# Performance work log

Hardware: AMD Instinct MI355X
Metric: run time of the kernel (lower is better)

## Reference

```python
import jax, jax.numpy as jnp
import numpy as np

B = 4096
IN_FEATS = 1024
OUT_FEATS = 1024
NUM_HEADS = 16
NUM_MEMS = 4096
HEAD_DIM = OUT_FEATS // NUM_HEADS
TEMPERATURE = 1.0
EPS = 0.0  # original code uses plain jnp.linalg.norm (no eps)


def setup_inputs() -> dict:
    key = jax.random.key(0)
    k1, k2, k3 = jax.random.split(key, 3)
    x = jax.random.normal(k1, (B, IN_FEATS), dtype=jnp.float32)
    # eqx.nn.Linear stores weight as [out, in]; uniform-like init replaced with normal scaled
    W_q = jax.random.normal(k2, (OUT_FEATS, IN_FEATS), dtype=jnp.float32) * (1.0 / np.sqrt(IN_FEATS))
    memories = jax.random.normal(k3, (NUM_HEADS, NUM_MEMS, HEAD_DIM), dtype=jnp.float32) * 0.02
    return {"x": x, "W_q": W_q, "memories": memories}


def reference(x, W_q, memories):
    # q = query_proj(x): [B, out_feats] -> [B, H, d]
    q = (x @ W_q.T).reshape(B, NUM_HEADS, HEAD_DIM)
    # L2-normalize queries and memories along feature dim
    q_norm = q / jnp.linalg.norm(q, axis=-1, keepdims=True)
    mem_norm = memories / jnp.linalg.norm(memories, axis=-1, keepdims=True)
    # cosine-similarity scores: [B, H, M]
    attn_scores = jnp.einsum('bhd,hmd->bhm', q_norm, mem_norm)
    # soft readout (hard=False branch)
    mem_probs = jax.nn.softmax(attn_scores / TEMPERATURE, axis=-1)
    # weighted combine of normalized memories, scaled by sqrt(head_dim)
    out = jnp.einsum('bhm,hmd->bhd', mem_probs, mem_norm) * jnp.sqrt(HEAD_DIM).astype(x.dtype)
    return out.reshape(B, OUT_FEATS)
```

## Files before the change

### kernel.cpp

```cpp
#include <hip/hip_runtime.h>
#include <stdint.h>

#define B_SZ  4096
#define HEADS 16
#define HD    64
#define M_SZ  4096
#define K_IN  1024
#define SW    72
#define LOG2E 1.44269504088896f

typedef _Float16 f16;
typedef f16  f16x4 __attribute__((ext_vector_type(4)));
typedef f16  f16x8 __attribute__((ext_vector_type(8)));
typedef float f32x4 __attribute__((ext_vector_type(4)));

union U8 { uint4 u4; f16x8 h8; unsigned int ui[4]; unsigned short us[8]; };

__device__ __forceinline__ unsigned short f2h(float f) {
    _Float16 h = (_Float16)f;
    return __builtin_bit_cast(unsigned short, h);
}
__device__ __forceinline__ f16x8 ldsv8(const unsigned short* p) {
    U8 u; u.u4 = *reinterpret_cast<const uint4*>(p); return u.h8;
}

#if __has_builtin(__builtin_amdgcn_exp2f)
#define EXP2F(x) __builtin_amdgcn_exp2f(x)
#else
#define EXP2F(x) __expf((x) * 0.6931471805599453f)
#endif

__device__ __forceinline__ void gload_lds16(const void* g, void* l) {
    __builtin_amdgcn_global_load_lds(
        (const __attribute__((address_space(1))) void*)g,
        (__attribute__((address_space(3))) void*)l, 16, 0, 0);
}

__global__ __launch_bounds__(256) void k_conv(const float* __restrict__ x,
                                              const float* __restrict__ Wq,
                                              unsigned short* __restrict__ xh,
                                              unsigned short* __restrict__ Wh) {
    const int b = blockIdx.x;
    const float* src;
    unsigned short* dst;
    size_t base;
    if (b < 2048) { src = x;  dst = xh; base = (size_t)b * 2048; }
    else          { src = Wq; dst = Wh; base = (size_t)(b - 2048) * 2048; }
    const size_t i = base + (size_t)threadIdx.x * 8;
    float4 f0 = reinterpret_cast<const float4*>(src + i)[0];
    float4 f1 = reinterpret_cast<const float4*>(src + i)[1];
    U8 u;
    u.us[0] = f2h(f0.x); u.us[1] = f2h(f0.y); u.us[2] = f2h(f0.z); u.us[3] = f2h(f0.w);
    u.us[4] = f2h(f1.x); u.us[5] = f2h(f1.y); u.us[6] = f2h(f1.z); u.us[7] = f2h(f1.w);
    *reinterpret_cast<uint4*>(dst + i) = u.u4;
}

__global__ __launch_bounds__(256) void k_prep_mem(const float* __restrict__ mem,
                                                  unsigned short* __restrict__ F) {
    __shared__ float part[64][4];
    __shared__ float scale[64];
    __shared__ unsigned short Tn[64 * SW];

    const int h  = blockIdx.y;
    const int tl = blockIdx.x;
    const int m0 = tl * 64;
    const int tid = threadIdx.x;
    const int r = tid >> 2;
    const int c = tid & 3;

    const float* src = mem + ((size_t)(h * M_SZ + m0 + r)) * HD + c * 16;
    float v[16];
    float ss = 0.f;
#pragma unroll
    for (int i = 0; i < 4; i++) {
        float4 f = reinterpret_cast<const float4*>(src)[i];
        v[4*i+0] = f.x; v[4*i+1] = f.y; v[4*i+2] = f.z; v[4*i+3] = f.w;
        ss += f.x*f.x + f.y*f.y + f.z*f.z + f.w*f.w;
    }
    part[r][c] = ss;
    __syncthreads();
    if (tid < 64) {
        float s = part[tid][0] + part[tid][1] + part[tid][2] + part[tid][3];
        scale[tid] = rsqrtf(s);
    }
    __syncthreads();
    const float sc = scale[r];

    U8 a, b;
#pragma unroll
    for (int i = 0; i < 8; i++) { a.us[i] = f2h(v[i] * sc); b.us[i] = f2h(v[8 + i] * sc); }
    *reinterpret_cast<uint4*>(&Tn[r * SW + c * 16])     = a.u4;
    *reinterpret_cast<uint4*>(&Tn[r * SW + c * 16 + 8]) = b.u4;
    __syncthreads();

    const int w = tid >> 6, lane = tid & 63;
    const int l15 = lane & 15, quad = lane >> 4;
    unsigned short* Fd = F + ((size_t)(h * 64 + tl) * 16) * 512;

#pragma unroll
    for (int i = 0; i < 2; i++) {
        const int ch = w * 2 + i, g = ch >> 1, s = ch & 1;
        const int mp = 32 * (g >> 1) + ((l15 >> 2) * 8) + 4 * (g & 1) + (l15 & 3);
        uint4 vv = *reinterpret_cast<const uint4*>(&Tn[mp * SW + s * 32 + quad * 8]);
        *reinterpret_cast<uint4*>(Fd + ch * 512 + lane * 8) = vv;
    }
#pragma unroll
    for (int i = 0; i < 2; i++) {
        const int c2 = w * 2 + i, p = c2 >> 2, n = c2 & 3;
        U8 u;
#pragma unroll
        for (int j = 0; j < 8; j++)
            u.us[j] = Tn[(32 * p + quad * 8 + j) * SW + n * 16 + l15];
        *reinterpret_cast<uint4*>(Fd + (8 + c2) * 512 + lane * 8) = u.u4;
    }
}

__global__ __launch_bounds__(256, 2) void k_qproj(const unsigned short* __restrict__ xh,
                                                  const unsigned short* __restrict__ Wh,
                                                  unsigned short* __restrict__ qn) {
    __shared__ unsigned short As[128 * SW];
    __shared__ unsigned short Bs[64 * SW];

    const int b0 = blockIdx.x * 128;
    const int n0 = blockIdx.y * 64;
    const int t = threadIdx.x;
    const int w = t >> 6, lane = t & 63;
    const int l15 = lane & 15, quad = lane >> 4;

    f32x4 acc[2][4] = {};

    for (int kb = 0; kb < K_IN; kb += 64) {
        __syncthreads();
        {
            const unsigned short* px = xh + (size_t)(b0 + (t >> 1)) * K_IN + kb + (t & 1) * 32;
            const unsigned short* pw = Wh + (size_t)(n0 + (t >> 2)) * K_IN + kb + (t & 3) * 16;
            uint4 av[4];
#pragma unroll
            for (int i = 0; i < 4; i++) av[i] = reinterpret_cast<const uint4*>(px)[i];
            uint4 bv[2];
#pragma unroll
            for (int i = 0; i < 2; i++) bv[i] = reinterpret_cast<const uint4*>(pw)[i];
#pragma unroll
            for (int i = 0; i < 4; i++)
                *reinterpret_cast<uint4*>(&As[(t >> 1) * SW + (t & 1) * 32 + i * 8]) = av[i];
#pragma unroll
            for (int i = 0; i < 2; i++)
                *reinterpret_cast<uint4*>(&Bs[(t >> 2) * SW + (t & 3) * 16 + i * 8]) = bv[i];
        }
        __syncthreads();

#pragma unroll
        for (int s = 0; s < 2; s++) {
            f16x8 af[2];
#pragma unroll
            for (int qg = 0; qg < 2; qg++)
                af[qg] = ldsv8(&As[(w * 32 + qg * 16 + l15) * SW + s * 32 + quad * 8]);
#pragma unroll
            for (int g = 0; g < 4; g++) {
                f16x8 bf_ = ldsv8(&Bs[(g * 16 + l15) * SW + s * 32 + quad * 8]);
#pragma unroll
                for (int qg = 0; qg < 2; qg++)
                    acc[qg][g] = __builtin_amdgcn_mfma_f32_16x16x32_f16(af[qg], bf_, acc[qg][g], 0, 0, 0);
            }
        }
    }

    __syncthreads();
    unsigned short* Ct = As;
#pragma unroll
    for (int qg = 0; qg < 2; qg++) {
        float ssq[4];
#pragma unroll
        for (int r = 0; r < 4; r++) {
            float s = 0.f;
#pragma unroll
            for (int g = 0; g < 4; g++) s += acc[qg][g][r] * acc[qg][g][r];
            ssq[r] = s;
        }
#pragma unroll
        for (int mask = 1; mask <= 8; mask <<= 1)
#pragma unroll
            for (int r = 0; r < 4; r++) ssq[r] += __shfl_xor(ssq[r], mask, 64);
#pragma unroll
        for (int r = 0; r < 4; r++) {
            float inv = rsqrtf(ssq[r]) * LOG2E;
#pragma unroll
            for (int g = 0; g < 4; g++)
                Ct[(w * 32 + qg * 16 + quad * 4 + r) * SW + g * 16 + l15] = f2h(acc[qg][g][r] * inv);
        }
    }
    __syncthreads();

    const int row = t >> 1, half = (t & 1) * 32;
    unsigned short* dq = qn + (size_t)(b0 + row) * 1024 + n0 + half;
#pragma unroll
    for (int i = 0; i < 4; i++)
        reinterpret_cast<uint4*>(dq)[i] = *reinterpret_cast<const uint4*>(&Ct[row * SW + half + i * 8]);
}

__global__ __launch_bounds__(256, 2) void k_attn(const unsigned short* __restrict__ qn,
                                                 const unsigned short* __restrict__ F,
                                                 float* __restrict__ out) {
    __shared__ unsigned short buf[2][8192];

    const int b = blockIdx.x;
    const int h  = 2 * (b & 7) + (b >> 8);
    const int b0 = ((b >> 3) & 31) * 128;
    const int t = threadIdx.x;
    const int w = t >> 6, lane = t & 63;
    const int l15 = lane & 15, quad = lane >> 4;

    f16x8 qf[2][2];
#pragma unroll
    for (int qg = 0; qg < 2; qg++)
#pragma unroll
        for (int s = 0; s < 2; s++) {
            U8 u;
            u.u4 = *reinterpret_cast<const uint4*>(
                qn + (size_t)(b0 + w * 32 + qg * 16 + l15) * 1024 + h * 64 + s * 32 + quad * 8);
            qf[qg][s] = u.h8;
        }

    const unsigned short* Fh = F + (size_t)h * 64 * 8192;

    f32x4 accO[2][4] = {};
    float lsum[2] = {0.f, 0.f};

    f16x8 puA[2][2], puB[2][2];
    f16x8 bwA[8],   bwB[8];

#pragma unroll
    for (int i = 0; i < 4; i++) {
        const int ch = w * 4 + i;
        gload_lds16(Fh + ch * 512 + lane * 8, &buf[0][ch * 512]);
    }
    __syncthreads();
    {
        f16x8 am[8];
#pragma unroll
        for (int ch = 0; ch < 8; ch++) am[ch] = ldsv8(&buf[0][ch * 512 + lane * 8]);
#pragma unroll
        for (int ch = 0; ch < 8; ch++) bwA[ch] = ldsv8(&buf[0][(8 + ch) * 512 + lane * 8]);
#pragma unroll
        for (int i = 0; i < 4; i++) {
            const int ch = w * 4 + i;
            gload_lds16(Fh + 8192 + ch * 512 + lane * 8, &buf[1][ch * 512]);
        }
#pragma unroll
        for (int g = 0; g < 4; g++) {
            const int qg = g >> 1, p = g & 1;
            f32x4 t0 = {0.f,0.f,0.f,0.f}, t1 = {0.f,0.f,0.f,0.f};
            t0 = __builtin_amdgcn_mfma_f32_16x16x32_f16(am[4*p+0], qf[qg][0], t0, 0, 0, 0);
            t0 = __builtin_amdgcn_mfma_f32_16x16x32_f16(am[4*p+1], qf[qg][1], t0, 0, 0, 0);
            t1 = __builtin_amdgcn_mfma_f32_16x16x32_f16(am[4*p+2], qf[qg][0], t1, 0, 0, 0);
            t1 = __builtin_amdgcn_mfma_f32_16x16x32_f16(am[4*p+3], qf[qg][1], t1, 0, 0, 0);
            float p0 = EXP2F(t0[0]), p1 = EXP2F(t0[1]), p2 = EXP2F(t0[2]), p3 = EXP2F(t0[3]);
            float p4 = EXP2F(t1[0]), p5 = EXP2F(t1[1]), p6 = EXP2F(t1[2]), p7 = EXP2F(t1[3]);
            lsum[qg] += ((p0 + p1) + (p2 + p3)) + ((p4 + p5) + (p6 + p7));
            U8 pu;
#if __has_builtin(__builtin_amdgcn_cvt_pkrtz)
            pu.ui[0] = __builtin_bit_cast(unsigned int, __builtin_amdgcn_cvt_pkrtz(p0, p1));
            pu.ui[1] = __builtin_bit_cast(unsigned int, __builtin_amdgcn_cvt_pkrtz(p2, p3));
            pu.ui[2] = __builtin_bit_cast(unsigned int, __builtin_amdgcn_cvt_pkrtz(p4, p5));
            pu.ui[3] = __builtin_bit_cast(unsigned int, __builtin_amdgcn_cvt_pkrtz(p6, p7));
#else
            pu.us[0]=f2h(p0); pu.us[1]=f2h(p1); pu.us[2]=f2h(p2); pu.us[3]=f2h(p3);
            pu.us[4]=f2h(p4); pu.us[5]=f2h(p5); pu.us[6]=f2h(p6); pu.us[7]=f2h(p7);
#endif
            puA[qg][p] = pu.h8;
        }
    }

    auto body = [&](int tl, f16x8 (&puC)[2][2], f16x8 (&bwC)[8],
                            f16x8 (&puN)[2][2], f16x8 (&bwN)[8]) {
        __syncthreads();
        const unsigned short* lb = buf[(tl + 1) & 1];
        f16x8 amn[8];
#pragma unroll
        for (int ch = 0; ch < 8; ch++) amn[ch] = ldsv8(&lb[ch * 512 + lane * 8]);
#pragma unroll
        for (int ch = 0; ch < 8; ch++) bwN[ch] = ldsv8(&lb[(8 + ch) * 512 + lane * 8]);
        if (tl + 2 < 64) {
            const unsigned short* gsrc = Fh + (size_t)(tl + 2) * 8192;
#pragma unroll
            for (int i = 0; i < 4; i++) {
                const int ch = w * 4 + i;
                gload_lds16(gsrc + ch * 512 + lane * 8, &buf[tl & 1][ch * 512]);
            }
        }

        f32x4 sa[4], sb[4];
        auto expPack = [&](int g) {
            const int qg = g >> 1, p = g & 1;
            float p0 = EXP2F(sa[g][0]), p1 = EXP2F(sa[g][1]), p2 = EXP2F(sa[g][2]), p3 = EXP2F(sa[g][3]);
            float p4 = EXP2F(sb[g][0]), p5 = EXP2F(sb[g][1]), p6 = EXP2F(sb[g][2]), p7 = EXP2F(sb[g][3]);
            lsum[qg] += ((p0 + p1) + (p2 + p3)) + ((p4 + p5) + (p6 + p7));
            U8 pu;
#if __has_builtin(__builtin_amdgcn_cvt_pkrtz)
            pu.ui[0] = __builtin_bit_cast(unsigned int, __builtin_amdgcn_cvt_pkrtz(p0, p1));
            pu.ui[1] = __builtin_bit_cast(unsigned int, __builtin_amdgcn_cvt_pkrtz(p2, p3));
            pu.ui[2] = __builtin_bit_cast(unsigned int, __builtin_amdgcn_cvt_pkrtz(p4, p5));
            pu.ui[3] = __builtin_bit_cast(unsigned int, __builtin_amdgcn_cvt_pkrtz(p6, p7));
#else
            pu.us[0]=f2h(p0); pu.us[1]=f2h(p1); pu.us[2]=f2h(p2); pu.us[3]=f2h(p3);
            pu.us[4]=f2h(p4); pu.us[5]=f2h(p5); pu.us[6]=f2h(p6); pu.us[7]=f2h(p7);
#endif
            puN[qg][p] = pu.h8;
        };

#pragma unroll
        for (int g = 0; g < 4; g++) {
            const int qg = g >> 1, p = g & 1;
            f32x4 t0 = {0.f,0.f,0.f,0.f}, t1 = {0.f,0.f,0.f,0.f};
            t0 = __builtin_amdgcn_mfma_f32_16x16x32_f16(amn[4*p+0], qf[qg][0], t0, 0, 0, 0);
            t0 = __builtin_amdgcn_mfma_f32_16x16x32_f16(amn[4*p+1], qf[qg][1], t0, 0, 0, 0);
            t1 = __builtin_amdgcn_mfma_f32_16x16x32_f16(amn[4*p+2], qf[qg][0], t1, 0, 0, 0);
            t1 = __builtin_amdgcn_mfma_f32_16x16x32_f16(amn[4*p+3], qf[qg][1], t1, 0, 0, 0);
            sa[g] = t0; sb[g] = t1;
#pragma unroll
            for (int n = 0; n < 4; n++)
                accO[qg][n] = __builtin_amdgcn_mfma_f32_16x16x32_f16(puC[qg][p], bwC[p * 4 + n], accO[qg][n], 0, 0, 0);
            if (g >= 1) expPack(g - 1);
        }
        expPack(3);
    };

    for (int tt = 0; tt < 31; ++tt) {
        body(2 * tt,     puA, bwA, puB, bwB);
        body(2 * tt + 1, puB, bwB, puA, bwA);
    }
    body(62, puA, bwA, puB, bwB);

#pragma unroll
    for (int g = 0; g < 4; g++) {
        const int qg = g >> 1, p = g & 1;
#pragma unroll
        for (int n = 0; n < 4; n++)
            accO[qg][n] = __builtin_amdgcn_mfma_f32_16x16x32_f16(puB[qg][p], bwB[p * 4 + n], accO[qg][n], 0, 0, 0);
    }

#pragma unroll
    for (int qg = 0; qg < 2; qg++) {
        float s = lsum[qg];
        s += __shfl_xor(s, 16, 64);
        s += __shfl_xor(s, 32, 64);
        float inv = 8.0f / s;
#pragma unroll
        for (int r = 0; r < 4; r++) {
            float iv = __shfl(inv, quad * 4 + r, 64);
            float* po = out + (size_t)(b0 + w * 32 + qg * 16 + quad * 4 + r) * 1024 + h * 64;
#pragma unroll
            for (int n = 0; n < 4; n++)
                po[n * 16 + l15] = accO[qg][n][r] * iv;
        }
    }
}

extern "C" void kernel_launch(void* const* d_in, const int* in_sizes, int n_in,
                              void* d_out, int out_size, void* d_ws, size_t ws_size,
                              hipStream_t stream) {
    (void)in_sizes; (void)n_in; (void)out_size; (void)ws_size;
    const float* x   = (const float*)d_in[0];
    const float* Wq  = (const float*)d_in[1];
    const float* mem = (const float*)d_in[2];
    float* out = (float*)d_out;

    unsigned short* qn = (unsigned short*)d_ws;
    unsigned short* F  = qn + (size_t)B_SZ * 1024;
    unsigned short* xh = F  + (size_t)HEADS * 64 * 16 * 512;
    unsigned short* Wh = xh + (size_t)B_SZ * K_IN;

    k_conv    <<<2560, 256, 0, stream>>>(x, Wq, xh, Wh);
    k_prep_mem<<<dim3(64, 16), 256, 0, stream>>>(mem, F);
    k_qproj   <<<dim3(32, 16), 256, 0, stream>>>(xh, Wh, qn);
    k_attn    <<<512, 256, 0, stream>>>(qn, F, out);
}
```

Measured before the change: 174.5 us.

## Use 8 waves per attention block with one 16-row query group each

The attention kernel now launches 512 threads per block instead of 256, and each wave handles 16 query rows instead of 32. Per-wave register state (accumulators, probabilities, query fragments) is halved. The F tile loads are spread over twice as many waves, and occupancy is raised via launch bounds (512, 4). The aim is more latency hiding through more concurrent waves. In exchange, every wave reloads the full F tile from LDS, so LDS read traffic per useful MFMA doubles, and the larger block synchronises more waves at each barrier.

After: 186.3 us. +6.8%, slower.

```diff
diff --git a/kernel.cpp b/kernel.cpp
--- a/kernel.cpp
+++ b/kernel.cpp
@@ -198,7 +198,7 @@
         reinterpret_cast<uint4*>(dq)[i] = *reinterpret_cast<const uint4*>(&Ct[row * SW + half + i * 8]);
 }
 
-__global__ __launch_bounds__(256, 2) void k_attn(const unsigned short* __restrict__ qn,
+__global__ __launch_bounds__(512, 4) void k_attn(const unsigned short* __restrict__ qn,
                                                  const unsigned short* __restrict__ F,
                                                  float* __restrict__ out) {
     __shared__ unsigned short buf[2][8192];
@@ -210,28 +210,26 @@
     const int w = t >> 6, lane = t & 63;
     const int l15 = lane & 15, quad = lane >> 4;
 
-    f16x8 qf[2][2];
-#pragma unroll
-    for (int qg = 0; qg < 2; qg++)
-#pragma unroll
-        for (int s = 0; s < 2; s++) {
-            U8 u;
-            u.u4 = *reinterpret_cast<const uint4*>(
-                qn + (size_t)(b0 + w * 32 + qg * 16 + l15) * 1024 + h * 64 + s * 32 + quad * 8);
-            qf[qg][s] = u.h8;
-        }
+    f16x8 qf[2];
+#pragma unroll
+    for (int s = 0; s < 2; s++) {
+        U8 u;
+        u.u4 = *reinterpret_cast<const uint4*>(
+            qn + (size_t)(b0 + w * 16 + l15) * 1024 + h * 64 + s * 32 + quad * 8);
+        qf[s] = u.h8;
+    }
 
     const unsigned short* Fh = F + (size_t)h * 64 * 8192;
 
-    f32x4 accO[2][4] = {};
-    float lsum[2] = {0.f, 0.f};
-
-    f16x8 puA[2][2], puB[2][2];
-    f16x8 bwA[8],   bwB[8];
-
-#pragma unroll
-    for (int i = 0; i < 4; i++) {
-        const int ch = w * 4 + i;
+    f32x4 accO[4] = {};
+    float lsum = 0.f;
+
+    f16x8 puA[2], puB[2];
+    f16x8 bwA[8], bwB[8];
+
+#pragma unroll
+    for (int i = 0; i < 2; i++) {
+        const int ch = w * 2 + i;
         gload_lds16(Fh + ch * 512 + lane * 8, &buf[0][ch * 512]);
     }
     __syncthreads();
@@ -242,21 +240,20 @@
 #pragma unroll
         for (int ch = 0; ch < 8; ch++) bwA[ch] = ldsv8(&buf[0][(8 + ch) * 512 + lane * 8]);
 #pragma unroll
-        for (int i = 0; i < 4; i++) {
-            const int ch = w * 4 + i;
+        for (int i = 0; i < 2; i++) {
+            const int ch = w * 2 + i;
             gload_lds16(Fh + 8192 + ch * 512 + lane * 8, &buf[1][ch * 512]);
         }
 #pragma unroll
-        for (int g = 0; g < 4; g++) {
-            const int qg = g >> 1, p = g & 1;
+        for (int p = 0; p < 2; p++) {
             f32x4 t0 = {0.f,0.f,0.f,0.f}, t1 = {0.f,0.f,0.f,0.f};
-            t0 = __builtin_amdgcn_mfma_f32_16x16x32_f16(am[4*p+0], qf[qg][0], t0, 0, 0, 0);
-            t0 = __builtin_amdgcn_mfma_f32_16x16x32_f16(am[4*p+1], qf[qg][1], t0, 0, 0, 0);
-            t1 = __builtin_amdgcn_mfma_f32_16x16x32_f16(am[4*p+2], qf[qg][0], t1, 0, 0, 0);
-            t1 = __builtin_amdgcn_mfma_f32_16x16x32_f16(am[4*p+3], qf[qg][1], t1, 0, 0, 0);
+            t0 = __builtin_amdgcn_mfma_f32_16x16x32_f16(am[4*p+0], qf[0], t0, 0, 0, 0);
+            t0 = __builtin_amdgcn_mfma_f32_16x16x32_f16(am[4*p+1], qf[1], t0, 0, 0, 0);
+            t1 = __builtin_amdgcn_mfma_f32_16x16x32_f16(am[4*p+2], qf[0], t1, 0, 0, 0);
+            t1 = __builtin_amdgcn_mfma_f32_16x16x32_f16(am[4*p+3], qf[1], t1, 0, 0, 0);
             float p0 = EXP2F(t0[0]), p1 = EXP2F(t0[1]), p2 = EXP2F(t0[2]), p3 = EXP2F(t0[3]);
             float p4 = EXP2F(t1[0]), p5 = EXP2F(t1[1]), p6 = EXP2F(t1[2]), p7 = EXP2F(t1[3]);
-            lsum[qg] += ((p0 + p1) + (p2 + p3)) + ((p4 + p5) + (p6 + p7));
+            lsum += ((p0 + p1) + (p2 + p3)) + ((p4 + p5) + (p6 + p7));
             U8 pu;
 #if __has_builtin(__builtin_amdgcn_cvt_pkrtz)
             pu.ui[0] = __builtin_bit_cast(unsigned int, __builtin_amdgcn_cvt_pkrtz(p0, p1));
@@ -267,12 +264,12 @@
             pu.us[0]=f2h(p0); pu.us[1]=f2h(p1); pu.us[2]=f2h(p2); pu.us[3]=f2h(p3);
             pu.us[4]=f2h(p4); pu.us[5]=f2h(p5); pu.us[6]=f2h(p6); pu.us[7]=f2h(p7);
 #endif
-            puA[qg][p] = pu.h8;
-        }
-    }
-
-    auto body = [&](int tl, f16x8 (&puC)[2][2], f16x8 (&bwC)[8],
-                            f16x8 (&puN)[2][2], f16x8 (&bwN)[8]) {
+            puA[p] = pu.h8;
+        }
+    }
+
+    auto body = [&](int tl, f16x8 (&puC)[2], f16x8 (&bwC)[8],
+                            f16x8 (&puN)[2], f16x8 (&bwN)[8]) {
         __syncthreads();
         const unsigned short* lb = buf[(tl + 1) & 1];
         f16x8 amn[8];
@@ -283,18 +280,17 @@
         if (tl + 2 < 64) {
             const unsigned short* gsrc = Fh + (size_t)(tl + 2) * 8192;
 #pragma unroll
-            for (int i = 0; i < 4; i++) {
-                const int ch = w * 4 + i;
+            for (int i = 0; i < 2; i++) {
+                const int ch = w * 2 + i;
                 gload_lds16(gsrc + ch * 512 + lane * 8, &buf[tl & 1][ch * 512]);
             }
         }
 
-        f32x4 sa[4], sb[4];
-        auto expPack = [&](int g) {
-            const int qg = g >> 1, p = g & 1;
-            float p0 = EXP2F(sa[g][0]), p1 = EXP2F(sa[g][1]), p2 = EXP2F(sa[g][2]), p3 = EXP2F(sa[g][3]);
-            float p4 = EXP2F(sb[g][0]), p5 = EXP2F(sb[g][1]), p6 = EXP2F(sb[g][2]), p7 = EXP2F(sb[g][3]);
-            lsum[qg] += ((p0 + p1) + (p2 + p3)) + ((p4 + p5) + (p6 + p7));
+        f32x4 sa[2], sb[2];
+        auto expPack = [&](int p) {
+            float p0 = EXP2F(sa[p][0]), p1 = EXP2F(sa[p][1]), p2 = EXP2F(sa[p][2]), p3 = EXP2F(sa[p][3]);
+            float p4 = EXP2F(sb[p][0]), p5 = EXP2F(sb[p][1]), p6 = EXP2F(sb[p][2]), p7 = EXP2F(sb[p][3]);
+            lsum += ((p0 + p1) + (p2 + p3)) + ((p4 + p5) + (p6 + p7));
             U8 pu;
 #if __has_builtin(__builtin_amdgcn_cvt_pkrtz)
             pu.ui[0] = __builtin_bit_cast(unsigned int, __builtin_amdgcn_cvt_pkrtz(p0, p1));
@@ -305,24 +301,23 @@
             pu.us[0]=f2h(p0); pu.us[1]=f2h(p1); pu.us[2]=f2h(p2); pu.us[3]=f2h(p3);
             pu.us[4]=f2h(p4); pu.us[5]=f2h(p5); pu.us[6]=f2h(p6); pu.us[7]=f2h(p7);
 #endif
-            puN[qg][p] = pu.h8;
+            puN[p] = pu.h8;
         };
 
 #pragma unroll
-        for (int g = 0; g < 4; g++) {
-            const int qg = g >> 1, p = g & 1;
+        for (int p = 0; p < 2; p++) {
             f32x4 t0 = {0.f,0.f,0.f,0.f}, t1 = {0.f,0.f,0.f,0.f};
-            t0 = __builtin_amdgcn_mfma_f32_16x16x32_f16(amn[4*p+0], qf[qg][0], t0, 0, 0, 0);
-            t0 = __builtin_amdgcn_mfma_f32_16x16x32_f16(amn[4*p+1], qf[qg][1], t0, 0, 0, 0);
-            t1 = __builtin_amdgcn_mfma_f32_16x16x32_f16(amn[4*p+2], qf[qg][0], t1, 0, 0, 0);
-            t1 = __builtin_amdgcn_mfma_f32_16x16x32_f16(amn[4*p+3], qf[qg][1], t1, 0, 0, 0);
-            sa[g] = t0; sb[g] = t1;
+            t0 = __builtin_amdgcn_mfma_f32_16x16x32_f16(amn[4*p+0], qf[0], t0, 0, 0, 0);
+            t0 = __builtin_amdgcn_mfma_f32_16x16x32_f16(amn[4*p+1], qf[1], t0, 0, 0, 0);
+            t1 = __builtin_amdgcn_mfma_f32_16x16x32_f16(amn[4*p+2], qf[0], t1, 0, 0, 0);
+            t1 = __builtin_amdgcn_mfma_f32_16x16x32_f16(amn[4*p+3], qf[1], t1, 0, 0, 0);
+            sa[p] = t0; sb[p] = t1;
 #pragma unroll
             for (int n = 0; n < 4; n++)
-                accO[qg][n] = __builtin_amdgcn_mfma_f32_16x16x32_f16(puC[qg][p], bwC[p * 4 + n], accO[qg][n], 0, 0, 0);
-            if (g >= 1) expPack(g - 1);
-        }
-        expPack(3);
+                accO[n] = __builtin_amdgcn_mfma_f32_16x16x32_f16(puC[p], bwC[p * 4 + n], accO[n], 0, 0, 0);
+            if (p >= 1) expPack(p - 1);
+        }
+        expPack(1);
     };
 
     for (int tt = 0; tt < 31; ++tt) {
@@ -332,26 +327,24 @@
     body(62, puA, bwA, puB, bwB);
 
 #pragma unroll
-    for (int g = 0; g < 4; g++) {
-        const int qg = g >> 1, p = g & 1;
+    for (int p = 0; p < 2; p++) {
 #pragma unroll
         for (int n = 0; n < 4; n++)
-            accO[qg][n] = __builtin_amdgcn_mfma_f32_16x16x32_f16(puB[qg][p], bwB[p * 4 + n], accO[qg][n], 0, 0, 0);
-    }
-
-#pragma unroll
-    for (int qg = 0; qg < 2; qg++) {
-        float s = lsum[qg];
+            accO[n] = __builtin_amdgcn_mfma_f32_16x16x32_f16(puB[p], bwB[p * 4 + n], accO[n], 0, 0, 0);
+    }
+
+    {
+        float s = lsum;
         s += __shfl_xor(s, 16, 64);
         s += __shfl_xor(s, 32, 64);
         float inv = 8.0f / s;
 #pragma unroll
         for (int r = 0; r < 4; r++) {
             float iv = __shfl(inv, quad * 4 + r, 64);
-            float* po = out + (size_t)(b0 + w * 32 + qg * 16 + quad * 4 + r) * 1024 + h * 64;
+            float* po = out + (size_t)(b0 + w * 16 + quad * 4 + r) * 1024 + h * 64;
 #pragma unroll
             for (int n = 0; n < 4; n++)
-                po[n * 16 + l15] = accO[qg][n][r] * iv;
+                po[n * 16 + l15] = accO[n][r] * iv;
         }
     }
 }
@@ -373,5 +366,5 @@
     k_conv    <<<2560, 256, 0, stream>>>(x, Wq, xh, Wh);
     k_prep_mem<<<dim3(64, 16), 256, 0, stream>>>(mem, F);
     k_qproj   <<<dim3(32, 16), 256, 0, stream>>>(xh, Wh, qn);
-    k_attn    <<<512, 256, 0, stream>>>(qn, F, out);
-}
+    k_attn    <<<512, 512, 0, stream>>>(qn, F, out);
+}
```

## Deepen LDS ring to four buffers and halve barriers in the attention loop

Applied to the files above, without the earlier changes.

The memory-tile staging grows from a double buffer to a four-slot ring that prefetches three tiles ahead. This lets the block barrier run once per pair of iterations instead of every iteration, cutting sync stalls and hiding global-load latency. It also raises wave priority around the MFMA group, feeds MFMAs a constant zero accumulator, and computes the softmax row sum from the packed fp16 probabilities with fdot2. The cost is double the LDS per block, and correctness now depends on the barrier spacing still covering the async load completion.

Result: no change. 175.3 us (+0.5%).

```diff
diff --git a/kernel.cpp b/kernel.cpp
--- a/kernel.cpp
+++ b/kernel.cpp
@@ -10,6 +10,7 @@
 #define LOG2E 1.44269504088896f
 
 typedef _Float16 f16;
+typedef f16  f16x2 __attribute__((ext_vector_type(2)));
 typedef f16  f16x4 __attribute__((ext_vector_type(4)));
 typedef f16  f16x8 __attribute__((ext_vector_type(8)));
 typedef float f32x4 __attribute__((ext_vector_type(4)));
@@ -201,7 +202,7 @@
 __global__ __launch_bounds__(256, 2) void k_attn(const unsigned short* __restrict__ qn,
                                                  const unsigned short* __restrict__ F,
                                                  float* __restrict__ out) {
-    __shared__ unsigned short buf[2][8192];
+    __shared__ unsigned short buf[4][8192];
 
     const int b = blockIdx.x;
     const int h  = 2 * (b & 7) + (b >> 8);
@@ -210,6 +211,8 @@
     const int w = t >> 6, lane = t & 63;
     const int l15 = lane & 15, quad = lane >> 4;
 
+    const f32x4 Z = {0.f, 0.f, 0.f, 0.f};
+
     f16x8 qf[2][2];
 #pragma unroll
     for (int qg = 0; qg < 2; qg++)
@@ -229,11 +232,35 @@
     f16x8 puA[2][2], puB[2][2];
     f16x8 bwA[8],   bwB[8];
 
-#pragma unroll
-    for (int i = 0; i < 4; i++) {
-        const int ch = w * 4 + i;
-        gload_lds16(Fh + ch * 512 + lane * 8, &buf[0][ch * 512]);
-    }
+#if __has_builtin(__builtin_amdgcn_fdot2)
+    const f16x2 one2 = {(_Float16)1.f, (_Float16)1.f};
+#define LSUM4(qgi, puv)                                                          \
+    {                                                                            \
+        float s_ = lsum[qgi];                                                    \
+        s_ = __builtin_amdgcn_fdot2(__builtin_bit_cast(f16x2, (puv).ui[0]), one2, s_, false); \
+        s_ = __builtin_amdgcn_fdot2(__builtin_bit_cast(f16x2, (puv).ui[1]), one2, s_, false); \
+        s_ = __builtin_amdgcn_fdot2(__builtin_bit_cast(f16x2, (puv).ui[2]), one2, s_, false); \
+        s_ = __builtin_amdgcn_fdot2(__builtin_bit_cast(f16x2, (puv).ui[3]), one2, s_, false); \
+        lsum[qgi] = s_;                                                          \
+    }
+#else
+#define LSUM4(qgi, puv)                                                          \
+    {                                                                            \
+        float a0 = (float)(puv).h8[0] + (float)(puv).h8[1];                      \
+        float a1 = (float)(puv).h8[2] + (float)(puv).h8[3];                      \
+        float a2 = (float)(puv).h8[4] + (float)(puv).h8[5];                      \
+        float a3 = (float)(puv).h8[6] + (float)(puv).h8[7];                      \
+        lsum[qgi] += (a0 + a1) + (a2 + a3);                                      \
+    }
+#endif
+
+#pragma unroll
+    for (int tp = 0; tp < 3; tp++)
+#pragma unroll
+        for (int i = 0; i < 4; i++) {
+            const int ch = w * 4 + i;
+            gload_lds16(Fh + (size_t)tp * 8192 + ch * 512 + lane * 8, &buf[tp][ch * 512]);
+        }
     __syncthreads();
     {
         f16x8 am[8];
@@ -242,21 +269,14 @@
 #pragma unroll
         for (int ch = 0; ch < 8; ch++) bwA[ch] = ldsv8(&buf[0][(8 + ch) * 512 + lane * 8]);
 #pragma unroll
-        for (int i = 0; i < 4; i++) {
-            const int ch = w * 4 + i;
-            gload_lds16(Fh + 8192 + ch * 512 + lane * 8, &buf[1][ch * 512]);
-        }
-#pragma unroll
         for (int g = 0; g < 4; g++) {
             const int qg = g >> 1, p = g & 1;
-            f32x4 t0 = {0.f,0.f,0.f,0.f}, t1 = {0.f,0.f,0.f,0.f};
-            t0 = __builtin_amdgcn_mfma_f32_16x16x32_f16(am[4*p+0], qf[qg][0], t0, 0, 0, 0);
+            f32x4 t0 = __builtin_amdgcn_mfma_f32_16x16x32_f16(am[4*p+0], qf[qg][0], Z, 0, 0, 0);
             t0 = __builtin_amdgcn_mfma_f32_16x16x32_f16(am[4*p+1], qf[qg][1], t0, 0, 0, 0);
-            t1 = __builtin_amdgcn_mfma_f32_16x16x32_f16(am[4*p+2], qf[qg][0], t1, 0, 0, 0);
+            f32x4 t1 = __builtin_amdgcn_mfma_f32_16x16x32_f16(am[4*p+2], qf[qg][0], Z, 0, 0, 0);
             t1 = __builtin_amdgcn_mfma_f32_16x16x32_f16(am[4*p+3], qf[qg][1], t1, 0, 0, 0);
             float p0 = EXP2F(t0[0]), p1 = EXP2F(t0[1]), p2 = EXP2F(t0[2]), p3 = EXP2F(t0[3]);
             float p4 = EXP2F(t1[0]), p5 = EXP2F(t1[1]), p6 = EXP2F(t1[2]), p7 = EXP2F(t1[3]);
-            lsum[qg] += ((p0 + p1) + (p2 + p3)) + ((p4 + p5) + (p6 + p7));
             U8 pu;
 #if __has_builtin(__builtin_amdgcn_cvt_pkrtz)
             pu.ui[0] = __builtin_bit_cast(unsigned int, __builtin_amdgcn_cvt_pkrtz(p0, p1));
@@ -267,25 +287,25 @@
             pu.us[0]=f2h(p0); pu.us[1]=f2h(p1); pu.us[2]=f2h(p2); pu.us[3]=f2h(p3);
             pu.us[4]=f2h(p4); pu.us[5]=f2h(p5); pu.us[6]=f2h(p6); pu.us[7]=f2h(p7);
 #endif
+            LSUM4(qg, pu);
             puA[qg][p] = pu.h8;
         }
     }
 
     auto body = [&](int tl, f16x8 (&puC)[2][2], f16x8 (&bwC)[8],
                             f16x8 (&puN)[2][2], f16x8 (&bwN)[8]) {
-        __syncthreads();
-        const unsigned short* lb = buf[(tl + 1) & 1];
+        const unsigned short* lb = buf[(tl + 1) & 3];
         f16x8 amn[8];
 #pragma unroll
         for (int ch = 0; ch < 8; ch++) amn[ch] = ldsv8(&lb[ch * 512 + lane * 8]);
 #pragma unroll
         for (int ch = 0; ch < 8; ch++) bwN[ch] = ldsv8(&lb[(8 + ch) * 512 + lane * 8]);
-        if (tl + 2 < 64) {
-            const unsigned short* gsrc = Fh + (size_t)(tl + 2) * 8192;
+        if (tl + 3 < 64) {
+            const unsigned short* gsrc = Fh + (size_t)(tl + 3) * 8192;
 #pragma unroll
             for (int i = 0; i < 4; i++) {
                 const int ch = w * 4 + i;
-                gload_lds16(gsrc + ch * 512 + lane * 8, &buf[tl & 1][ch * 512]);
+                gload_lds16(gsrc + ch * 512 + lane * 8, &buf[(tl + 3) & 3][ch * 512]);
             }
         }
 
@@ -294,7 +314,6 @@
             const int qg = g >> 1, p = g & 1;
             float p0 = EXP2F(sa[g][0]), p1 = EXP2F(sa[g][1]), p2 = EXP2F(sa[g][2]), p3 = EXP2F(sa[g][3]);
             float p4 = EXP2F(sb[g][0]), p5 = EXP2F(sb[g][1]), p6 = EXP2F(sb[g][2]), p7 = EXP2F(sb[g][3]);
-            lsum[qg] += ((p0 + p1) + (p2 + p3)) + ((p4 + p5) + (p6 + p7));
             U8 pu;
 #if __has_builtin(__builtin_amdgcn_cvt_pkrtz)
             pu.ui[0] = __builtin_bit_cast(unsigned int, __builtin_amdgcn_cvt_pkrtz(p0, p1));
@@ -305,30 +324,34 @@
             pu.us[0]=f2h(p0); pu.us[1]=f2h(p1); pu.us[2]=f2h(p2); pu.us[3]=f2h(p3);
             pu.us[4]=f2h(p4); pu.us[5]=f2h(p5); pu.us[6]=f2h(p6); pu.us[7]=f2h(p7);
 #endif
+            LSUM4(qg, pu);
             puN[qg][p] = pu.h8;
         };
 
 #pragma unroll
         for (int g = 0; g < 4; g++) {
             const int qg = g >> 1, p = g & 1;
-            f32x4 t0 = {0.f,0.f,0.f,0.f}, t1 = {0.f,0.f,0.f,0.f};
-            t0 = __builtin_amdgcn_mfma_f32_16x16x32_f16(amn[4*p+0], qf[qg][0], t0, 0, 0, 0);
+            __builtin_amdgcn_s_setprio(1);
+            f32x4 t0 = __builtin_amdgcn_mfma_f32_16x16x32_f16(amn[4*p+0], qf[qg][0], Z, 0, 0, 0);
             t0 = __builtin_amdgcn_mfma_f32_16x16x32_f16(amn[4*p+1], qf[qg][1], t0, 0, 0, 0);
-            t1 = __builtin_amdgcn_mfma_f32_16x16x32_f16(amn[4*p+2], qf[qg][0], t1, 0, 0, 0);
+            f32x4 t1 = __builtin_amdgcn_mfma_f32_16x16x32_f16(amn[4*p+2], qf[qg][0], Z, 0, 0, 0);
             t1 = __builtin_amdgcn_mfma_f32_16x16x32_f16(amn[4*p+3], qf[qg][1], t1, 0, 0, 0);
             sa[g] = t0; sb[g] = t1;
 #pragma unroll
             for (int n = 0; n < 4; n++)
                 accO[qg][n] = __builtin_amdgcn_mfma_f32_16x16x32_f16(puC[qg][p], bwC[p * 4 + n], accO[qg][n], 0, 0, 0);
+            __builtin_amdgcn_s_setprio(0);
             if (g >= 1) expPack(g - 1);
         }
         expPack(3);
     };
 
     for (int tt = 0; tt < 31; ++tt) {
+        __syncthreads();
         body(2 * tt,     puA, bwA, puB, bwB);
         body(2 * tt + 1, puB, bwB, puA, bwA);
     }
+    __syncthreads();
     body(62, puA, bwA, puB, bwB);
 
 #pragma unroll
```
